# Kernel tuning notes

Measured on AMD Instinct MI355X. Metric: run time of the kernel, lower is better.

## Reference

```python
import jax, jax.numpy as jnp
import numpy as np

NMIX = 10  # mixtures in discretized mix of logistics


def _causal_mask(kh, kw, include_center):
    # rows strictly above center fully visible; center row left of center; optionally center
    m = np.zeros((kh, kw), dtype=np.float32)
    m[: kh // 2, :] = 1.0
    m[kh // 2, : kw // 2] = 1.0
    if include_center:
        m[kh // 2, kw // 2] = 1.0
    return jnp.asarray(m)[None, None]  # [1,1,kh,kw] broadcast over O,I


def _conv(x, w):
    return jax.lax.conv_general_dilated(
        x, w, (1, 1), 'SAME', dimension_numbers=('NCHW', 'OIHW', 'NCHW'))


def pixelcnn_params(x, w_in, w_blk, w_out1, w_out2):
    mA = _causal_mask(7, 7, False)
    mB = _causal_mask(3, 3, True)
    h = _conv(x, w_in * mA)                      # [B,160,H,W]
    for i in range(w_blk.shape[0]):              # 5 gated resnet blocks
        g = _conv(jax.nn.relu(h), w_blk[i] * mB)  # [B,320,H,W]
        a, b = jnp.split(g, 2, axis=1)
        h = h + jnp.tanh(a) * jax.nn.sigmoid(b)
    h = jax.nn.relu(_conv(jax.nn.relu(h), w_out1))
    return _conv(h, w_out2)                      # [B,100,H,W]


def dmol_log_prob(x, params):
    # x: [B,3,H,W] in [-1,1]; params: [B,100,H,W]; returns per-example log prob [B]
    B, C, H, W = x.shape
    l = jnp.transpose(params, (0, 2, 3, 1))       # [B,H,W,100]
    xt = jnp.transpose(x, (0, 2, 3, 1))           # [B,H,W,3]
    logit_probs = l[..., :NMIX]                   # [B,H,W,10]
    rest = l[..., NMIX:].reshape(B, H, W, 3, 3 * NMIX)
    means = rest[..., :NMIX]
    log_scales = jnp.maximum(rest[..., NMIX:2 * NMIX], -7.0)
    coeffs = jnp.tanh(rest[..., 2 * NMIX:])
    xe = xt[..., None]                            # [B,H,W,3,1]
    m1 = means[..., 0, :]
    m2 = means[..., 1, :] + coeffs[..., 0, :] * xe[..., 0, :]
    m3 = means[..., 2, :] + coeffs[..., 1, :] * xe[..., 0, :] + coeffs[..., 2, :] * xe[..., 1, :]
    means_adj = jnp.stack([m1, m2, m3], axis=3)   # [B,H,W,3,10]
    centered = xe - means_adj
    inv_stdv = jnp.exp(-log_scales)
    plus_in = inv_stdv * (centered + 1.0 / 255.0)
    min_in = inv_stdv * (centered - 1.0 / 255.0)
    cdf_delta = jax.nn.sigmoid(plus_in) - jax.nn.sigmoid(min_in)
    log_cdf_plus = plus_in - jax.nn.softplus(plus_in)
    log_one_minus_cdf_min = -jax.nn.softplus(min_in)
    mid_in = inv_stdv * centered
    log_pdf_mid = mid_in - log_scales - 2.0 * jax.nn.softplus(mid_in)
    log_prob_in = jnp.where(cdf_delta > 1e-5,
                            jnp.log(jnp.clip(cdf_delta, 1e-12, None)),
                            log_pdf_mid - np.float32(np.log(127.5)))
    log_probs_c = jnp.where(xe < -0.999, log_cdf_plus,
                            jnp.where(xe > 0.999, log_one_minus_cdf_min, log_prob_in))
    log_probs = jnp.sum(log_probs_c, axis=3) + jax.nn.log_softmax(logit_probs, axis=-1)
    lp = jax.scipy.special.logsumexp(log_probs, axis=-1)  # [B,H,W]
    return jnp.sum(lp, axis=(1, 2))                       # [B]


def setup_inputs() -> dict:
    key = jax.random.key(0)
    ks = jax.random.split(key, 5)
    F = 160
    return {
        'samples': jax.random.uniform(ks[0], (16, 3, 64, 64), dtype=jnp.float32),
        'w_in': jax.random.normal(ks[1], (F, 3, 7, 7), dtype=jnp.float32) * 0.05,
        'w_blk': jax.random.normal(ks[2], (5, 2 * F, F, 3, 3), dtype=jnp.float32) * 0.03,
        'w_out1': jax.random.normal(ks[3], (F, F, 1, 1), dtype=jnp.float32) * 0.05,
        'w_out2': jax.random.normal(ks[4], (100, F, 1, 1), dtype=jnp.float32) * 0.05,
    }


def reference(samples, w_in, w_blk, w_out1, w_out2):
    x = samples * 2.0 - 1.0
    params = pixelcnn_params(x, w_in, w_blk, w_out1, w_out2)
    return dmol_log_prob(x, params)
```

## Files before the change

### kernel.cpp

```cpp
#include <hip/hip_runtime.h>
#include <math.h>


using short8  = __attribute__((ext_vector_type(8))) short;
using short4v = __attribute__((ext_vector_type(4))) short;
using f32x4   = __attribute__((ext_vector_type(4))) float;

static constexpr float L2E = 1.44269504088896f;
static constexpr float LN2 = 0.69314718055995f;

__device__ __forceinline__ float fexp2(float x) { return __builtin_amdgcn_exp2f(x); }
__device__ __forceinline__ float flog2(float x) { return __builtin_amdgcn_logf(x); }
__device__ __forceinline__ float frcp(float x)  { return __builtin_amdgcn_rcpf(x); }
__device__ __forceinline__ float fexp(float x)  { return fexp2(x * L2E); }
__device__ __forceinline__ float flog(float x)  { return flog2(x) * LN2; }
__device__ __forceinline__ float fsigmoid(float x) { return frcp(1.f + fexp2(-x * L2E)); }
__device__ __forceinline__ float ftanh(float x)    { return 1.f - 2.f * frcp(1.f + fexp2(x * (2.f * L2E))); }
__device__ __forceinline__ float fsoftplus(float z) {
    float e = fexp2(-fabsf(z) * L2E);
    return fmaxf(z, 0.f) + flog2(1.f + e) * LN2;
}

__device__ __forceinline__ unsigned pk_bf16(float a, float b) {
    union { float f; unsigned u; } ua, ub; ua.f = a; ub.f = b;
    return __builtin_amdgcn_perm(ub.u + 0x7fffu, ua.u + 0x7fffu, 0x07060302u);
}

__device__ __forceinline__ short f2bf(float f) {
    union { float f; unsigned u; } v; v.f = f;
    unsigned r = (v.u + 0x7fffu + ((v.u >> 16) & 1u)) >> 16;
    return (short)r;
}

__device__ __forceinline__ float bf2f(unsigned short s) {
    union { unsigned u; float f; } v; v.u = ((unsigned)s) << 16; return v.f;
}

__device__ __forceinline__ unsigned relu2(unsigned v) {
    unsigned m = ((v & 0x80008000u) >> 15) * 0xffffu;
    return v & ~m;
}

static constexpr size_t X_OFF    = 0;
static constexpr size_t WINP_OFF = 786432;
static constexpr size_t W1P_OFF  = 817152;
static constexpr size_t W2P_OFF  = 868352;
static constexpr size_t WPB_OFF  = 919552;
static constexpr size_t HA_OFF   = 3479552;
static constexpr size_t HB_OFF   = 24451072;

__global__ void k_prep(const float* __restrict__ s, float* __restrict__ x, int n) {
    int i = blockIdx.x * 256 + threadIdx.x;
    if (i < n) x[i] = 2.f * s[i] - 1.f;
}

__global__ void k_twb(const float* __restrict__ w, short* __restrict__ wP) {
    int idx = blockIdx.x * 256 + threadIdx.x;
    if (idx >= 5 * 25 * 320 * 32) return;
    int icl = idx & 31;
    int oc  = (idx >> 5) % 320;
    int kt  = ((idx >> 5) / 320) % 25;
    int i   = idx / (25 * 320 * 32);
    int tap = kt / 5, ic = (kt % 5) * 32 + icl;
    const int ky[5] = {0,0,0,1,1}, kx[5] = {0,1,2,0,1};
    float v = w[(((size_t)(i * 320 + oc) * 160 + ic) * 3 + ky[tap]) * 3 + kx[tap]];
    wP[idx] = f2bf(v);
}

__global__ void k_twin(const float* __restrict__ w, short* __restrict__ wP) {
    int idx = blockIdx.x * 256 + threadIdx.x;
    if (idx >= 3 * 160 * 32) return;
    int icl = idx & 31;
    int oc  = (idx >> 5) % 160;
    int kc  = idx / 5120;
    int k = kc * 32 + icl;
    short v = 0;
    if (k < 72) {
        int tap = k / 3, ic = k % 3;
        int ky = (tap < 21) ? tap / 7 : 3;
        int kx = (tap < 21) ? tap % 7 : tap - 21;
        v = f2bf(w[((oc * 3 + ic) * 7 + ky) * 7 + kx]);
    }
    wP[idx] = v;
}

__global__ void k_tw1(const float* __restrict__ w, short* __restrict__ wP) {
    int idx = blockIdx.x * 256 + threadIdx.x;
    if (idx >= 5 * 160 * 32) return;
    int icl = idx & 31;
    int oc  = (idx >> 5) % 160;
    int kc  = idx / 5120;
    wP[idx] = f2bf(w[oc * 160 + kc * 32 + icl]);
}

__global__ void k_tw2(const float* __restrict__ w, short* __restrict__ wP) {
    int idx = blockIdx.x * 256 + threadIdx.x;
    if (idx >= 5 * 160 * 32) return;
    int icl = idx & 31;
    int oc  = (idx >> 5) % 160;
    int kc  = idx / 5120;
    wP[idx] = (oc < 100) ? f2bf(w[oc * 160 + kc * 32 + icl]) : (short)0;
}

__global__ __launch_bounds__(320) void k_convin(const float* __restrict__ X,
                                                const short* __restrict__ WINP,
                                                unsigned short* __restrict__ hout) {
    __shared__ float xls[3 * 4 * 40];
    __shared__ short Bls[32 * 104];
    int y = blockIdx.x >> 1, half = blockIdx.x & 1, b = blockIdx.y;
    int xbase = half * 32;
    int t = threadIdx.x;
    for (int i = t; i < 456; i += 320) {
        int col = i % 38; int r = (i / 38) % 4; int ic = i / 152;
        int xg = xbase + col - 3, yg = y + r - 3;
        float v = 0.f;
        if (xg >= 0 && xg < 64 && yg >= 0)
            v = X[((size_t)(b * 3 + ic) * 64 + yg) * 64 + xg];
        xls[(ic * 4 + r) * 40 + col] = v;
    }
    __syncthreads();
    for (int i = t; i < 3072; i += 320) {
        int k = i % 96; int px = i / 96;
        short v = 0;
        if (k < 72) {
            int tap = k / 3, ic = k % 3;
            int ky = (tap < 21) ? tap / 7 : 3;
            int kx = (tap < 21) ? tap % 7 : tap - 21;
            v = f2bf(xls[(ic * 4 + ky) * 40 + px + kx]);
        }
        Bls[px * 104 + k] = v;
    }
    __syncthreads();
    int lane = t & 63, w = t >> 6;
    int lx = lane & 15, q = lane >> 4;
    f32x4 acc[2][2] = {};
    const short* wl = WINP + lx * 32 + q * 8;
    #pragma unroll
    for (int kc = 0; kc < 3; ++kc) {
        short8 aF[2], bF[2];
        aF[0] = *(const short8*)(wl + (kc * 160 + 32 * w) * 32);
        aF[1] = *(const short8*)(wl + (kc * 160 + 32 * w + 16) * 32);
        #pragma unroll
        for (int nt = 0; nt < 2; ++nt)
            bF[nt] = *(const short8*)&Bls[(nt * 16 + lx) * 104 + kc * 32 + q * 8];
        #pragma unroll
        for (int mt = 0; mt < 2; ++mt)
            #pragma unroll
            for (int nt = 0; nt < 2; ++nt)
                acc[mt][nt] = __builtin_amdgcn_mfma_f32_16x16x32_bf16(
                    aF[mt], bF[nt], acc[mt][nt], 0, 0, 0);
    }
    size_t rowbase = ((size_t)(b * 64 + y)) * 64 * 160;
    #pragma unroll
    for (int mt = 0; mt < 2; ++mt) {
        int c0 = 32 * w + mt * 16 + q * 4;
        #pragma unroll
        for (int nt = 0; nt < 2; ++nt) {
            int px = xbase + nt * 16 + lx;
            uint2 o;
            o.x = pk_bf16(acc[mt][nt][0], acc[mt][nt][1]);
            o.y = pk_bf16(acc[mt][nt][2], acc[mt][nt][3]);
            *(uint2*)&hout[rowbase + (size_t)px * 160 + c0] = o;
        }
    }
}

__global__ __launch_bounds__(320) void k_blk(const unsigned short* __restrict__ hin,
                                             unsigned short* __restrict__ hout,
                                             const short* __restrict__ wP) {
    __shared__ short in_s[2 * 34 * 168];
    int y = blockIdx.x >> 1, half = blockIdx.x & 1, b = blockIdx.y;
    int xbase = half * 32;
    int t = threadIdx.x;
    for (int i = t; i < 1360; i += 320) {
        int c8 = i % 20; int xl = (i / 20) % 34; int r = i / 680;
        int xg = xbase + xl - 1, yg = y + r - 1;
        uint4 v = {0u, 0u, 0u, 0u};
        if (xg >= 0 && xg < 64 && yg >= 0) {
            v = *(const uint4*)&hin[(((size_t)(b * 64 + yg)) * 64 + xg) * 160 + c8 * 8];
            v.x = relu2(v.x); v.y = relu2(v.y); v.z = relu2(v.z); v.w = relu2(v.w);
        }
        *(uint4*)&in_s[(r * 34 + xl) * 168 + c8 * 8] = v;
    }
    __syncthreads();

    int lane = t & 63, w = t >> 6;
    int lx = lane & 15, q = lane >> 4;
    f32x4 acc[4][2] = {};
    const short* wl = wP + lx * 32 + q * 8;
    const int dxs[5] = {-1, 0, 1, -1, 0};
    const int rws[5] = {0, 0, 0, 1, 1};
    #pragma unroll
    for (int tap = 0; tap < 5; ++tap) {
        int rb0 = (rws[tap] * 34 + 1 + dxs[tap] + lx) * 168 + q * 8;
        #pragma unroll
        for (int k5 = 0; k5 < 5; ++k5) {
            const short* wk = wl + (tap * 5 + k5) * 10240;
            short8 aF[4], bF[2];
            aF[0] = *(const short8*)(wk + (32 * w) * 32);
            aF[1] = *(const short8*)(wk + (32 * w + 16) * 32);
            aF[2] = *(const short8*)(wk + (160 + 32 * w) * 32);
            aF[3] = *(const short8*)(wk + (176 + 32 * w) * 32);
            int rb = rb0 + k5 * 32;
            bF[0] = *(const short8*)&in_s[rb];
            bF[1] = *(const short8*)&in_s[rb + 16 * 168];
            #pragma unroll
            for (int mt = 0; mt < 4; ++mt)
                #pragma unroll
                for (int nt = 0; nt < 2; ++nt)
                    acc[mt][nt] = __builtin_amdgcn_mfma_f32_16x16x32_bf16(
                        aF[mt], bF[nt], acc[mt][nt], 0, 0, 0);
        }
    }
    size_t rowbase = ((size_t)(b * 64 + y)) * 64 * 160;
    #pragma unroll
    for (int mt = 0; mt < 2; ++mt) {
        int c0 = 32 * w + mt * 16 + q * 4;
        #pragma unroll
        for (int nt = 0; nt < 2; ++nt) {
            int px = xbase + nt * 16 + lx;
            size_t off = rowbase + (size_t)px * 160 + c0;
            ushort4 hv = *(const ushort4*)&hin[off];
            float o0 = bf2f(hv.x) + ftanh(acc[mt][nt][0]) * fsigmoid(acc[mt + 2][nt][0]);
            float o1 = bf2f(hv.y) + ftanh(acc[mt][nt][1]) * fsigmoid(acc[mt + 2][nt][1]);
            float o2 = bf2f(hv.z) + ftanh(acc[mt][nt][2]) * fsigmoid(acc[mt + 2][nt][2]);
            float o3 = bf2f(hv.w) + ftanh(acc[mt][nt][3]) * fsigmoid(acc[mt + 2][nt][3]);
            uint2 o;
            o.x = pk_bf16(o0, o1);
            o.y = pk_bf16(o2, o3);
            *(uint2*)&hout[off] = o;
        }
    }
}

__global__ __launch_bounds__(320) void k_head(const unsigned short* __restrict__ hin,
                                              const short* __restrict__ W1P,
                                              const short* __restrict__ W2P,
                                              const float* __restrict__ X,
                                              float* __restrict__ out) {
    __shared__ char arena[14848];
    __shared__ short h2ls[32 * 168];
    short* hls = (short*)arena;
    float* Pls = (float*)arena;
    float* lpls = (float*)(arena + 13312);
    int y = blockIdx.x >> 1, half = blockIdx.x & 1, b = blockIdx.y;
    int xbase = half * 32;
    int t = threadIdx.x;
    size_t rowbase = ((size_t)(b * 64 + y)) * 64 * 160;
    for (int i = t; i < 640; i += 320) {
        int c8 = i % 20; int px = i / 20;
        uint4 v = *(const uint4*)&hin[rowbase + (size_t)(xbase + px) * 160 + c8 * 8];
        v.x = relu2(v.x); v.y = relu2(v.y); v.z = relu2(v.z); v.w = relu2(v.w);
        *(uint4*)&hls[px * 168 + c8 * 8] = v;
    }
    __syncthreads();
    int lane = t & 63, w = t >> 6;
    int lx = lane & 15, q = lane >> 4;
    {
        f32x4 acc[2][2] = {};
        const short* wl = W1P + lx * 32 + q * 8;
        #pragma unroll
        for (int kc = 0; kc < 5; ++kc) {
            short8 aF[2], bF[2];
            aF[0] = *(const short8*)(wl + (kc * 160 + 32 * w) * 32);
            aF[1] = *(const short8*)(wl + (kc * 160 + 32 * w + 16) * 32);
            #pragma unroll
            for (int nt = 0; nt < 2; ++nt)
                bF[nt] = *(const short8*)&hls[(nt * 16 + lx) * 168 + kc * 32 + q * 8];
            #pragma unroll
            for (int mt = 0; mt < 2; ++mt)
                #pragma unroll
                for (int nt = 0; nt < 2; ++nt)
                    acc[mt][nt] = __builtin_amdgcn_mfma_f32_16x16x32_bf16(
                        aF[mt], bF[nt], acc[mt][nt], 0, 0, 0);
        }
        __syncthreads();
        #pragma unroll
        for (int mt = 0; mt < 2; ++mt) {
            int c0 = 32 * w + mt * 16 + q * 4;
            #pragma unroll
            for (int nt = 0; nt < 2; ++nt) {
                int px = nt * 16 + lx;
                union { short4v s; unsigned u[2]; } sv;
                sv.u[0] = pk_bf16(fmaxf(acc[mt][nt][0], 0.f), fmaxf(acc[mt][nt][1], 0.f));
                sv.u[1] = pk_bf16(fmaxf(acc[mt][nt][2], 0.f), fmaxf(acc[mt][nt][3], 0.f));
                *(short4v*)&h2ls[px * 168 + c0] = sv.s;
            }
        }
    }
    __syncthreads();
    {
        f32x4 acc[2][2] = {};
        const short* wl = W2P + lx * 32 + q * 8;
        #pragma unroll
        for (int kc = 0; kc < 5; ++kc) {
            short8 aF[2], bF[2];
            aF[0] = *(const short8*)(wl + (kc * 160 + 32 * w) * 32);
            aF[1] = *(const short8*)(wl + (kc * 160 + 32 * w + 16) * 32);
            #pragma unroll
            for (int nt = 0; nt < 2; ++nt)
                bF[nt] = *(const short8*)&h2ls[(nt * 16 + lx) * 168 + kc * 32 + q * 8];
            #pragma unroll
            for (int mt = 0; mt < 2; ++mt)
                #pragma unroll
                for (int nt = 0; nt < 2; ++nt)
                    acc[mt][nt] = __builtin_amdgcn_mfma_f32_16x16x32_bf16(
                        aF[mt], bF[nt], acc[mt][nt], 0, 0, 0);
        }
        #pragma unroll
        for (int mt = 0; mt < 2; ++mt) {
            int c0 = 32 * w + mt * 16 + q * 4;
            if (c0 < 100) {
                #pragma unroll
                for (int nt = 0; nt < 2; ++nt) {
                    int px = nt * 16 + lx;
                    float4 o;
                    o.x = acc[mt][nt][0]; o.y = acc[mt][nt][1];
                    o.z = acc[mt][nt][2]; o.w = acc[mt][nt][3];
                    *(float4*)&Pls[px * 104 + c0] = o;
                }
            }
        }
    }
    __syncthreads();
    const float LOG127P5 = 4.8481163504f;
    {
        int px = t & 31, m = t >> 5;
        const float* pp = &Pls[px * 104];
        float xs[3];
        #pragma unroll
        for (int c = 0; c < 3; ++c)
            xs[c] = X[((size_t)(b * 3 + c)) * 4096 + (size_t)y * 64 + xbase + px];
        float mx = pp[0];
        #pragma unroll
        for (int j = 1; j < 10; ++j) mx = fmaxf(mx, pp[j]);
        float se = 0.f;
        #pragma unroll
        for (int j = 0; j < 10; ++j) se += fexp(pp[j] - mx);
        float lse = mx + flog(se);
        float sum = pp[m] - lse;
        float mean0 = pp[10 + m];
        float mean1 = pp[40 + m];
        float mean2 = pp[70 + m];
        float ls0 = fmaxf(pp[20 + m], -7.f);
        float ls1 = fmaxf(pp[50 + m], -7.f);
        float ls2 = fmaxf(pp[80 + m], -7.f);
        float c0 = ftanh(pp[30 + m]);
        float c1 = ftanh(pp[60 + m]);
        float c2 = ftanh(pp[90 + m]);
        float mu[3], lsv[3];
        mu[0] = mean0;
        mu[1] = mean1 + c0 * xs[0];
        mu[2] = mean2 + c1 * xs[0] + c2 * xs[1];
        lsv[0] = ls0; lsv[1] = ls1; lsv[2] = ls2;
        #pragma unroll
        for (int ci = 0; ci < 3; ++ci) {
            float cent = xs[ci] - mu[ci];
            float inv = fexp(-lsv[ci]);
            float plus_in = inv * (cent + 1.f / 255.f);
            float min_in = inv * (cent - 1.f / 255.f);
            float cdf_delta = fsigmoid(plus_in) - fsigmoid(min_in);
            float log_cdf_plus = plus_in - fsoftplus(plus_in);
            float log_om_cdf = -fsoftplus(min_in);
            float mid = inv * cent;
            float log_pdf_mid = mid - lsv[ci] - 2.f * fsoftplus(mid);
            float lpi = (cdf_delta > 1e-5f) ? flog(fmaxf(cdf_delta, 1e-12f))
                                            : (log_pdf_mid - LOG127P5);
            float lpc = (xs[ci] < -0.999f) ? log_cdf_plus
                       : ((xs[ci] > 0.999f) ? log_om_cdf : lpi);
            sum += lpc;
        }
        lpls[px * 12 + m] = sum;
    }
    __syncthreads();
    if (t < 32) {
        int px = t;
        float mx2 = lpls[px * 12];
        #pragma unroll
        for (int m = 1; m < 10; ++m) mx2 = fmaxf(mx2, lpls[px * 12 + m]);
        float se2 = 0.f;
        #pragma unroll
        for (int m = 0; m < 10; ++m) se2 += fexp(lpls[px * 12 + m] - mx2);
        float lp = mx2 + flog(se2);
        lp += __shfl_down(lp, 16, 32);
        lp += __shfl_down(lp, 8, 32);
        lp += __shfl_down(lp, 4, 32);
        lp += __shfl_down(lp, 2, 32);
        lp += __shfl_down(lp, 1, 32);
        if (t == 0) atomicAdd(&out[b], lp);
    }
}

extern "C" void kernel_launch(void* const* d_in, const int* in_sizes, int n_in,
                              void* d_out, int out_size, void* d_ws, size_t ws_size,
                              hipStream_t stream) {
    const float* samples = (const float*)d_in[0];
    const float* w_in    = (const float*)d_in[1];
    const float* w_blk   = (const float*)d_in[2];
    const float* w_out1  = (const float*)d_in[3];
    const float* w_out2  = (const float*)d_in[4];
    char* ws = (char*)d_ws;
    float* X    = (float*)(ws + X_OFF);
    short* WINP = (short*)(ws + WINP_OFF);
    short* W1P  = (short*)(ws + W1P_OFF);
    short* W2P  = (short*)(ws + W2P_OFF);
    short* WPB  = (short*)(ws + WPB_OFF);
    unsigned short* HA = (unsigned short*)(ws + HA_OFF);
    unsigned short* HB = (unsigned short*)(ws + HB_OFF);
    float* fout = (float*)d_out;

    k_prep<<<768, 256, 0, stream>>>(samples, X, 16 * 3 * 4096);
    k_twb<<<5000, 256, 0, stream>>>(w_blk, WPB);
    k_twin<<<60, 256, 0, stream>>>(w_in, WINP);
    k_tw1<<<100, 256, 0, stream>>>(w_out1, W1P);
    k_tw2<<<100, 256, 0, stream>>>(w_out2, W2P);

    k_convin<<<dim3(128, 16), 320, 0, stream>>>(X, WINP, HA);

    unsigned short* a = HA; unsigned short* bq = HB;
    for (int i = 0; i < 5; i++) {
        k_blk<<<dim3(128, 16), 320, 0, stream>>>(a, bq, WPB + (size_t)i * 25 * 320 * 32);
        unsigned short* tmp = a; a = bq; bq = tmp;
    }
    hipMemsetAsync(d_out, 0, (size_t)out_size * sizeof(float), stream);
    k_head<<<dim3(128, 16), 320, 0, stream>>>(a, W1P, W2P, X, fout);
}
```

Measured before the change: 540.0 us.

## Retile gated block conv to two full rows per workgroup with wider N reuse

Each k_blk workgroup now covers two full 64-pixel rows with 640 threads. Each wave owns 16 output channels plus their matching gate channels and computes 8 pixel tiles, instead of 32 channel pairs over 2 tiles. The aim is to reuse every global weight fragment across four times as many MFMAs and to cut the halo overhead of staging input in LDS. In exchange the grid drops to 512 workgroups and LDS use rises to a larger 3x66 tile. The row padding of 168 becomes 160, which may add LDS bank conflicts on the B-fragment reads.

```diff
diff --git a/kernel.cpp b/kernel.cpp
--- a/kernel.cpp
+++ b/kernel.cpp
@@ -165,71 +165,67 @@
     }
 }
 
-__global__ __launch_bounds__(320) void k_blk(const unsigned short* __restrict__ hin,
+__global__ __launch_bounds__(640) void k_blk(const unsigned short* __restrict__ hin,
                                              unsigned short* __restrict__ hout,
                                              const short* __restrict__ wP) {
-    __shared__ short in_s[2 * 34 * 168];
-    int y = blockIdx.x >> 1, half = blockIdx.x & 1, b = blockIdx.y;
-    int xbase = half * 32;
+    __shared__ short in_s[3 * 66 * 160];
+    int y0 = blockIdx.x * 2, b = blockIdx.y;
     int t = threadIdx.x;
-    for (int i = t; i < 1360; i += 320) {
-        int c8 = i % 20; int xl = (i / 20) % 34; int r = i / 680;
-        int xg = xbase + xl - 1, yg = y + r - 1;
+    for (int i = t; i < 3960; i += 640) {
+        int c8 = i % 20; int xl = (i / 20) % 66; int r = i / 1320;
+        int xg = xl - 1, yg = y0 + r - 1;
         uint4 v = {0u, 0u, 0u, 0u};
         if (xg >= 0 && xg < 64 && yg >= 0) {
             v = *(const uint4*)&hin[(((size_t)(b * 64 + yg)) * 64 + xg) * 160 + c8 * 8];
             v.x = relu2(v.x); v.y = relu2(v.y); v.z = relu2(v.z); v.w = relu2(v.w);
         }
-        *(uint4*)&in_s[(r * 34 + xl) * 168 + c8 * 8] = v;
-    }
-    __syncthreads();
-
-    int lane = t & 63, w = t >> 6;
+        *(uint4*)&in_s[(r * 66 + xl) * 160 + c8 * 8] = v;
+    }
+    __syncthreads();
+
+    int lane = t & 63, j = t >> 6;
     int lx = lane & 15, q = lane >> 4;
-    f32x4 acc[4][2] = {};
+    f32x4 acc[2][8] = {};
     const short* wl = wP + lx * 32 + q * 8;
     const int dxs[5] = {-1, 0, 1, -1, 0};
     const int rws[5] = {0, 0, 0, 1, 1};
     #pragma unroll
     for (int tap = 0; tap < 5; ++tap) {
-        int rb0 = (rws[tap] * 34 + 1 + dxs[tap] + lx) * 168 + q * 8;
         #pragma unroll
         for (int k5 = 0; k5 < 5; ++k5) {
             const short* wk = wl + (tap * 5 + k5) * 10240;
-            short8 aF[4], bF[2];
-            aF[0] = *(const short8*)(wk + (32 * w) * 32);
-            aF[1] = *(const short8*)(wk + (32 * w + 16) * 32);
-            aF[2] = *(const short8*)(wk + (160 + 32 * w) * 32);
-            aF[3] = *(const short8*)(wk + (176 + 32 * w) * 32);
-            int rb = rb0 + k5 * 32;
-            bF[0] = *(const short8*)&in_s[rb];
-            bF[1] = *(const short8*)&in_s[rb + 16 * 168];
-            #pragma unroll
-            for (int mt = 0; mt < 4; ++mt)
+            short8 aF[2], bF[8];
+            aF[0] = *(const short8*)(wk + (16 * j) * 32);
+            aF[1] = *(const short8*)(wk + (160 + 16 * j) * 32);
+            #pragma unroll
+            for (int nt = 0; nt < 8; ++nt) {
+                int rr = rws[tap] + (nt >> 2);
+                int xc = 1 + dxs[tap] + (nt & 3) * 16 + lx;
+                bF[nt] = *(const short8*)&in_s[(rr * 66 + xc) * 160 + k5 * 32 + q * 8];
+            }
+            #pragma unroll
+            for (int mt = 0; mt < 2; ++mt)
                 #pragma unroll
-                for (int nt = 0; nt < 2; ++nt)
+                for (int nt = 0; nt < 8; ++nt)
                     acc[mt][nt] = __builtin_amdgcn_mfma_f32_16x16x32_bf16(
                         aF[mt], bF[nt], acc[mt][nt], 0, 0, 0);
         }
     }
-    size_t rowbase = ((size_t)(b * 64 + y)) * 64 * 160;
+    int c0 = 16 * j + q * 4;
     #pragma unroll
-    for (int mt = 0; mt < 2; ++mt) {
-        int c0 = 32 * w + mt * 16 + q * 4;
-        #pragma unroll
-        for (int nt = 0; nt < 2; ++nt) {
-            int px = xbase + nt * 16 + lx;
-            size_t off = rowbase + (size_t)px * 160 + c0;
-            ushort4 hv = *(const ushort4*)&hin[off];
-            float o0 = bf2f(hv.x) + ftanh(acc[mt][nt][0]) * fsigmoid(acc[mt + 2][nt][0]);
-            float o1 = bf2f(hv.y) + ftanh(acc[mt][nt][1]) * fsigmoid(acc[mt + 2][nt][1]);
-            float o2 = bf2f(hv.z) + ftanh(acc[mt][nt][2]) * fsigmoid(acc[mt + 2][nt][2]);
-            float o3 = bf2f(hv.w) + ftanh(acc[mt][nt][3]) * fsigmoid(acc[mt + 2][nt][3]);
-            uint2 o;
-            o.x = pk_bf16(o0, o1);
-            o.y = pk_bf16(o2, o3);
-            *(uint2*)&hout[off] = o;
-        }
+    for (int nt = 0; nt < 8; ++nt) {
+        int y = y0 + (nt >> 2);
+        int px = (nt & 3) * 16 + lx;
+        size_t off = (((size_t)(b * 64 + y)) * 64 + px) * 160 + c0;
+        ushort4 hv = *(const ushort4*)&hin[off];
+        float o0 = bf2f(hv.x) + ftanh(acc[0][nt][0]) * fsigmoid(acc[1][nt][0]);
+        float o1 = bf2f(hv.y) + ftanh(acc[0][nt][1]) * fsigmoid(acc[1][nt][1]);
+        float o2 = bf2f(hv.z) + ftanh(acc[0][nt][2]) * fsigmoid(acc[1][nt][2]);
+        float o3 = bf2f(hv.w) + ftanh(acc[0][nt][3]) * fsigmoid(acc[1][nt][3]);
+        uint2 o;
+        o.x = pk_bf16(o0, o1);
+        o.y = pk_bf16(o2, o3);
+        *(uint2*)&hout[off] = o;
     }
 }
 
@@ -419,7 +415,7 @@
 
     unsigned short* a = HA; unsigned short* bq = HB;
     for (int i = 0; i < 5; i++) {
-        k_blk<<<dim3(128, 16), 320, 0, stream>>>(a, bq, WPB + (size_t)i * 25 * 320 * 32);
+        k_blk<<<dim3(32, 16), 640, 0, stream>>>(a, bq, WPB + (size_t)i * 25 * 320 * 32);
         unsigned short* tmp = a; a = bq; bq = tmp;
     }
     hipMemsetAsync(d_out, 0, (size_t)out_size * sizeof(float), stream);
```

Result: no change. 542.9 us (+0.5%).
